# Optimization experiments

Hardware: AMD Instinct MI355X
Metric: run time of the kernel (lower is better)

The kernel has to match this reference:

```python
import jax, jax.numpy as jnp
import numpy as np

HEADS = 4

def _axial_attn(xs, wqkv, wproj, bproj, heads=HEADS):
    # xs: [B', C, L]; wqkv: [3C, C]; wproj: [C, C]; bproj: [C]
    Bp, C, L = xs.shape
    hd = C // heads
    scale = hd ** -0.5
    qkv = jnp.einsum('oc,bcl->bol', wqkv, xs)  # [B', 3C, L]
    q, k, v = jnp.split(qkv, 3, axis=1)
    q = q.reshape(Bp, heads, hd, L)
    k = k.reshape(Bp, heads, hd, L)
    v = v.reshape(Bp, heads, hd, L)
    attn = jax.nn.softmax(jnp.einsum('bhdi,bhdj->bhij', q, k) * scale, axis=-1)
    out = jnp.einsum('bhij,bhdj->bhdi', attn, v).reshape(Bp, C, L)
    return jnp.einsum('oc,bcl->bol', wproj, out) + bproj[None, :, None]

def setup_inputs() -> dict:
    key = jax.random.key(0)
    ks = jax.random.split(key, 7)
    B, C, H, W = 8, 128, 128, 128
    return {
        'x': jax.random.normal(ks[0], (B, C, H, W), dtype=jnp.float32),
        'wqkv_h': jax.random.normal(ks[1], (3 * C, C), dtype=jnp.float32) * 0.05,
        'wproj_h': jax.random.normal(ks[2], (C, C), dtype=jnp.float32) * 0.05,
        'bproj_h': jax.random.normal(ks[3], (C,), dtype=jnp.float32) * 0.05,
        'wqkv_w': jax.random.normal(ks[4], (3 * C, C), dtype=jnp.float32) * 0.05,
        'wproj_w': jax.random.normal(ks[5], (C, C), dtype=jnp.float32) * 0.05,
        'bproj_w': jax.random.normal(ks[6], (C,), dtype=jnp.float32) * 0.05,
    }

def reference(x, wqkv_h, wproj_h, bproj_h, wqkv_w, wproj_w, bproj_w):
    B, C, H, W = x.shape
    # height pass: rows become batch, attend along W
    xh = x.transpose(0, 2, 1, 3).reshape(B * H, C, W)
    xh = _axial_attn(xh, wqkv_h, wproj_h, bproj_h)
    xh = xh.reshape(B, H, C, W).transpose(0, 2, 1, 3)
    # width pass: cols become batch, attend along H
    xw = x.transpose(0, 3, 1, 2).reshape(B * W, C, H)
    xw = _axial_attn(xw, wqkv_w, wproj_w, bproj_w)
    xw = xw.reshape(B, W, C, H).transpose(0, 2, 3, 1)
    return (xh + xw) / 2
```

## Files before the change

### kernel.cpp

```cpp
#include <hip/hip_runtime.h>
#include <hip/hip_bf16.h>
#include <stdint.h>

typedef __attribute__((ext_vector_type(8))) short short8v;
typedef __attribute__((ext_vector_type(4))) float f32x4;
typedef unsigned short u16;
typedef unsigned int u32;

__device__ __align__(16) u16 g_xh [8u * 128u * 128u * 128u];
__device__ __align__(16) u16 g_xTw[8u * 128u * 128u * 128u];
__device__ __align__(16) u16 g_W1 [8u * 128u * 128u * 128u];
__device__ __align__(16) u16 g_W2 [8u * 128u * 128u * 128u];
__device__ __align__(16) u16 g_wqkvP[2u * 49152u];
__device__ __align__(16) u16 g_wpP [2u * 16384u];

#define XST_OFF 0
#define QT_OFF  32768
#define KT_OFF  43008
#define VH_OFF  53248
#define OT_OFF  61952
#define SMEM_BYTES 72192

__device__ __forceinline__ u16 f2bf(float f) {
    u32 b = __float_as_uint(f);
    b += 0x7FFFu + ((b >> 16) & 1u);
    return (u16)(b >> 16);
}
__device__ __forceinline__ u32 pk2(float a, float b) {
    __hip_bfloat162 h = __float22bfloat162_rn(make_float2(a, b));
    union { __hip_bfloat162 h; u32 u; } cv; cv.h = h; return cv.u;
}
__device__ __forceinline__ float bf2f(u16 u) {
    return __uint_as_float(((u32)u) << 16);
}

__global__ __launch_bounds__(512)
void prep_weights(const float* __restrict__ wqkv_h, const float* __restrict__ wproj_h,
                  const float* __restrict__ wqkv_w, const float* __restrict__ wproj_w)
{
    const float QSC = 0.17677669529663687f * 1.4426950408889634f;
    int id = blockIdx.x * 512 + threadIdx.x;
    if (id < 12288) {
        int p = id / 6144, i2 = id % 6144;
        int h = i2 / 1536, i3 = i2 % 1536;
        int t = i3 / 256,  i4 = i3 % 256;
        int kk = i4 / 64,  lane = i4 % 64;
        int cc = lane & 15, qq = lane >> 4;
        int r96 = t * 16 + cc;
        int g = r96 >> 5, rl = r96 & 31;
        const float* src = (p == 0 ? wqkv_h : wqkv_w) + (g * 128 + h * 32 + rl) * 128 + kk * 32 + qq * 8;
        float4 a = *(const float4*)src;
        float4 c = *(const float4*)(src + 4);
        float s = (g == 0) ? QSC : 1.0f;
        *(uint4*)(g_wqkvP + (size_t)id * 8) =
            make_uint4(pk2(a.x * s, a.y * s), pk2(a.z * s, a.w * s),
                       pk2(c.x * s, c.y * s), pk2(c.z * s, c.w * s));
    } else {
        int id2 = id - 12288;
        int p = id2 / 2048, i2 = id2 % 2048;
        int h = i2 / 512,  i3 = i2 % 512;
        int t = i3 / 64,   lane = i3 % 64;
        int cc = lane & 15, qq = lane >> 4;
        int o = t * 16 + cc;
        const float* src = (p == 0 ? wproj_h : wproj_w) + o * 128 + h * 32 + qq * 8;
        float4 a = *(const float4*)src;
        float4 c = *(const float4*)(src + 4);
        *(uint4*)(g_wpP + (size_t)id2 * 8) =
            make_uint4(pk2(a.x * 0.5f, a.y * 0.5f), pk2(a.z * 0.5f, a.w * 0.5f),
                       pk2(c.x * 0.5f, c.y * 0.5f), pk2(c.z * 0.5f, c.w * 0.5f));
    }
}

__global__ __launch_bounds__(256)
void transpose_x(const float* __restrict__ x)
{
    __shared__ char tsm[32768];
    const int b = blockIdx.x >> 6;
    const int hp = blockIdx.x & 63;
    const int tid = threadIdx.x;
    for (int hh = 0; hh < 2; ++hh) {
        const int h = hp * 2 + hh;
        #pragma unroll
        for (int it = 0; it < 16; ++it) {
            int task = it * 256 + tid;
            int w = task & 127, c4 = task >> 7;
            const float* p = x + (size_t)b * 2097152 + (c4 * 4) * 16384 + h * 128 + w;
            u32 u0 = pk2(p[0], p[16384]);
            u32 u1 = pk2(p[2 * 16384], p[3 * 16384]);
            int off = w * 256 + ((((c4 >> 1) << 4) ^ ((w & 7) << 4)) | ((c4 & 1) << 3));
            *(uint2*)(tsm + off) = make_uint2(u0, u1);
        }
        __syncthreads();
        #pragma unroll
        for (int it = 0; it < 8; ++it) {
            int i = it * 256 + tid;
            *(uint4*)(g_xh + (size_t)(b * 128 + h) * 16384 + i * 8) = *(const uint4*)(tsm + i * 16);
        }
        #pragma unroll
        for (int it = 0; it < 8; ++it) {
            int i = it * 256 + tid;
            int w = i >> 4, c8 = i & 15;
            uint4 v = *(const uint4*)(tsm + w * 256 + ((c8 << 4) ^ ((w & 7) << 4)));
            size_t ds = ((size_t)(b * 128 + w) * 128 + h) * 128 + (((c8 << 4) ^ ((h & 7) << 4)) >> 1);
            *(uint4*)(g_xTw + ds) = v;
        }
        __syncthreads();
    }
}

__global__ __launch_bounds__(512, 4)
void attn_kernel(const float* __restrict__ bias_h, const float* __restrict__ bias_w)
{
    extern __shared__ char smem[];
    const int t    = threadIdx.x;
    const int lane = t & 63;
    const int wv   = t >> 6;
    const int cc   = lane & 15;
    const int qq   = lane >> 4;
    const int pass = blockIdx.x >> 10;
    const int b    = (blockIdx.x >> 7) & 7;
    const int row  = blockIdx.x & 127;
    const f32x4 zf4 = (f32x4){0.f, 0.f, 0.f, 0.f};

    {
        const u16* slab = (pass ? g_xTw : g_xh) + (size_t)(b * 128 + row) * 16384;
        #pragma unroll
        for (int it = 0; it < 4; ++it) {
            int idx = t + 512 * it;
            *(uint4*)(smem + XST_OFF + idx * 16) = *(const uint4*)(slab + idx * 8);
        }
    }

    const float* bias = pass ? bias_w : bias_h;
    float biasr[4];
    #pragma unroll
    for (int r = 0; r < 4; ++r) biasr[r] = bias[wv * 16 + 4 * qq + r] * 0.5f;

    f32x4 yacc[8];
    #pragma unroll
    for (int i = 0; i < 8; ++i) yacc[i] = zf4;

    __syncthreads();

    const int og = wv & 1;
    const int lg = wv >> 1;

    for (int h = 0; h < 4; ++h) {
        const u16* wb  = g_wqkvP + (size_t)(pass * 4 + h) * 12288;
        const u16* wpb = g_wpP   + (size_t)(pass * 4 + h) * 4096 + (wv * 64 + lane) * 8;

        {
            f32x4 acc[3][2];
            #pragma unroll
            for (int ot = 0; ot < 3; ++ot)
                #pragma unroll
                for (int lt = 0; lt < 2; ++lt) acc[ot][lt] = zf4;
            __builtin_amdgcn_s_setprio(1);
            #pragma unroll
            for (int kk = 0; kk < 4; ++kk) {
                short8v A[3], Bf[2];
                #pragma unroll
                for (int ot = 0; ot < 3; ++ot)
                    A[ot] = *(const short8v*)(wb + (((og * 3 + ot) * 4 + kk) * 64 + lane) * 8);
                #pragma unroll
                for (int lt = 0; lt < 2; ++lt) {
                    int l = lg * 32 + lt * 16 + cc;
                    Bf[lt] = *(const short8v*)(smem + XST_OFF + l * 256 + (((kk * 64 + qq * 16)) ^ ((l & 7) << 4)));
                }
                #pragma unroll
                for (int ot = 0; ot < 3; ++ot)
                    #pragma unroll
                    for (int lt = 0; lt < 2; ++lt)
                        acc[ot][lt] = __builtin_amdgcn_mfma_f32_16x16x32_bf16(A[ot], Bf[lt], acc[ot][lt], 0, 0, 0);
            }
            __builtin_amdgcn_s_setprio(0);
            #pragma unroll
            for (int ot = 0; ot < 3; ++ot) {
                int got = og * 3 + ot;
                #pragma unroll
                for (int lt = 0; lt < 2; ++lt) {
                    int l0 = (lg * 2 + lt) * 16 + cc;
                    f32x4 v = acc[ot][lt];
                    if (got < 2) {
                        *(uint2*)(smem + QT_OFF + l0 * 80 + (got * 16 + 4 * qq) * 2) =
                            make_uint2(pk2(v[0], v[1]), pk2(v[2], v[3]));
                    } else if (got < 4) {
                        *(uint2*)(smem + KT_OFF + l0 * 80 + ((got - 2) * 16 + 4 * qq) * 2) =
                            make_uint2(pk2(v[0], v[1]), pk2(v[2], v[3]));
                    } else {
                        int d0 = (got - 4) * 16 + 4 * qq;
                        #pragma unroll
                        for (int r = 0; r < 4; ++r)
                            *(u16*)(smem + VH_OFF + (d0 + r) * 272 + l0 * 2) = f2bf(v[r]);
                    }
                }
            }
        }
        __syncthreads();

        f32x4 sacc[8];
        {
            short8v aq = *(const short8v*)(smem + QT_OFF + (wv * 16 + cc) * 80 + qq * 16);
            __builtin_amdgcn_s_setprio(1);
            #pragma unroll
            for (int jt = 0; jt < 8; ++jt) {
                short8v bk = *(const short8v*)(smem + KT_OFF + (jt * 16 + cc) * 80 + qq * 16);
                sacc[jt] = __builtin_amdgcn_mfma_f32_16x16x32_bf16(bk, aq, zf4, 0, 0, 0);
            }
            __builtin_amdgcn_s_setprio(0);
        }
        float mx = -3.4e38f;
        #pragma unroll
        for (int jt = 0; jt < 8; ++jt)
            #pragma unroll
            for (int r = 0; r < 4; ++r) mx = fmaxf(mx, sacc[jt][r]);
        mx = fmaxf(mx, __shfl_xor(mx, 16));
        mx = fmaxf(mx, __shfl_xor(mx, 32));
        float sm = 0.f;
        #pragma unroll
        for (int jt = 0; jt < 8; ++jt)
            #pragma unroll
            for (int r = 0; r < 4; ++r) {
                float p = exp2f(sacc[jt][r] - mx);
                sacc[jt][r] = p;
                sm += p;
            }
        sm += __shfl_xor(sm, 16);
        sm += __shfl_xor(sm, 32);
        float rden = 1.0f / sm;
        u32 u[8][2];
        #pragma unroll
        for (int jt = 0; jt < 8; ++jt) {
            u[jt][0] = pk2(sacc[jt][0], sacc[jt][1]);
            u[jt][1] = pk2(sacc[jt][2], sacc[jt][3]);
        }

        f32x4 oacc[2] = {zf4, zf4};
        const int base = cc + ((qq & 1) << 5);
        const bool hiT = (qq >> 1) != 0;
        __builtin_amdgcn_s_setprio(1);
        #pragma unroll
        for (int kt = 0; kt < 4; ++kt) {
            int a0 = __shfl((int)u[2 * kt][0], base),      a1 = __shfl((int)u[2 * kt][1], base);
            int a2 = __shfl((int)u[2 * kt][0], base + 16), a3 = __shfl((int)u[2 * kt][1], base + 16);
            int b0 = __shfl((int)u[2 * kt + 1][0], base),      b1 = __shfl((int)u[2 * kt + 1][1], base);
            int b2 = __shfl((int)u[2 * kt + 1][0], base + 16), b3 = __shfl((int)u[2 * kt + 1][1], base + 16);
            union { uint4 u4; short8v s8; } pf;
            pf.u4 = make_uint4((u32)(hiT ? b0 : a0), (u32)(hiT ? b1 : a1),
                               (u32)(hiT ? b2 : a2), (u32)(hiT ? b3 : a3));
            #pragma unroll
            for (int dt = 0; dt < 2; ++dt) {
                short8v vf = *(const short8v*)(smem + VH_OFF + (dt * 16 + cc) * 272 + kt * 64 + qq * 16);
                oacc[dt] = __builtin_amdgcn_mfma_f32_16x16x32_bf16(vf, pf.s8, oacc[dt], 0, 0, 0);
            }
        }
        __builtin_amdgcn_s_setprio(0);
        #pragma unroll
        for (int dt = 0; dt < 2; ++dt) {
            *(uint2*)(smem + OT_OFF + (wv * 16 + cc) * 80 + (dt * 16 + 4 * qq) * 2) =
                make_uint2(pk2(oacc[dt][0] * rden, oacc[dt][1] * rden),
                           pk2(oacc[dt][2] * rden, oacc[dt][3] * rden));
        }
        __syncthreads();

        {
            short8v aw = *(const short8v*)wpb;
            __builtin_amdgcn_s_setprio(1);
            #pragma unroll
            for (int it = 0; it < 8; ++it) {
                short8v of = *(const short8v*)(smem + OT_OFF + (it * 16 + cc) * 80 + qq * 16);
                yacc[it] = __builtin_amdgcn_mfma_f32_16x16x32_bf16(aw, of, yacc[it], 0, 0, 0);
            }
            __builtin_amdgcn_s_setprio(0);
        }
    }

    u16* dst = pass ? g_W2 : g_W1;
    #pragma unroll
    for (int it = 0; it < 8; ++it) {
        int l = it * 16 + cc;
        u32 p01 = pk2(yacc[it][0] + biasr[0], yacc[it][1] + biasr[1]);
        u32 p23 = pk2(yacc[it][2] + biasr[2], yacc[it][3] + biasr[3]);
        int o0 = wv * 16 + 4 * qq;
        size_t idx = ((size_t)(b * 128 + o0) * 128 + row) * 128 + l;
        dst[idx]         = (u16)p01;
        dst[idx + 16384] = (u16)(p01 >> 16);
        dst[idx + 32768] = (u16)p23;
        dst[idx + 49152] = (u16)(p23 >> 16);
    }
}

__global__ __launch_bounds__(256)
void merge_w(float* __restrict__ out)
{
    __shared__ char msm[128 * 264];
    const int b = blockIdx.x >> 7;
    const int o = blockIdx.x & 127;
    const int tid = threadIdx.x;
    const u16* slab = g_W2 + (size_t)(b * 128 + o) * 16384;
    #pragma unroll
    for (int it = 0; it < 8; ++it) {
        int i = it * 256 + tid;
        int w = i >> 4, h8 = i & 15;
        *(uint4*)(msm + w * 264 + h8 * 16) = *(const uint4*)(slab + w * 128 + h8 * 8);
    }
    __syncthreads();
    const u16* w1p = g_W1 + (size_t)(b * 128 + o) * 16384;
    float* op = out + (size_t)(b * 128 + o) * 16384;
    #pragma unroll
    for (int it = 0; it < 8; ++it) {
        int i = it * 256 + tid;
        int h = i >> 4, w8 = i & 15;
        uint4 w1 = *(const uint4*)(w1p + h * 128 + w8 * 8);
        float f[8];
        #pragma unroll
        for (int k = 0; k < 8; ++k)
            f[k] = bf2f(*(const u16*)(msm + (w8 * 8 + k) * 264 + h * 2));
        float* dp = op + h * 128 + w8 * 8;
        float4 v0, v1;
        v0.x = f[0] + bf2f((u16)(w1.x & 0xFFFF));
        v0.y = f[1] + bf2f((u16)(w1.x >> 16));
        v0.z = f[2] + bf2f((u16)(w1.y & 0xFFFF));
        v0.w = f[3] + bf2f((u16)(w1.y >> 16));
        v1.x = f[4] + bf2f((u16)(w1.z & 0xFFFF));
        v1.y = f[5] + bf2f((u16)(w1.z >> 16));
        v1.z = f[6] + bf2f((u16)(w1.w & 0xFFFF));
        v1.w = f[7] + bf2f((u16)(w1.w >> 16));
        *(float4*)dp = v0;
        *(float4*)(dp + 4) = v1;
    }
}

extern "C" void kernel_launch(void* const* d_in, const int* in_sizes, int n_in,
                              void* d_out, int out_size, void* d_ws, size_t ws_size,
                              hipStream_t stream)
{
    const float* x       = (const float*)d_in[0];
    const float* wqkv_h  = (const float*)d_in[1];
    const float* wproj_h = (const float*)d_in[2];
    const float* bproj_h = (const float*)d_in[3];
    const float* wqkv_w  = (const float*)d_in[4];
    const float* wproj_w = (const float*)d_in[5];
    const float* bproj_w = (const float*)d_in[6];
    float* out = (float*)d_out;

    (void)hipFuncSetAttribute((const void*)attn_kernel,
                              hipFuncAttributeMaxDynamicSharedMemorySize, SMEM_BYTES);

    prep_weights<<<dim3(32), dim3(512), 0, stream>>>(wqkv_h, wproj_h, wqkv_w, wproj_w);
    transpose_x<<<dim3(512), dim3(256), 0, stream>>>(x);
    attn_kernel<<<dim3(2048), dim3(512), SMEM_BYTES, stream>>>(bproj_h, bproj_w);
    merge_w<<<dim3(1024), dim3(256), 0, stream>>>(out);
}
```

Measured before the change: 168.2 us.

## Keep attention output in registers for projection, drop LDS staging buffer

The per-head attention output is no longer written to an LDS tile and read back across waves. Each wave now shuffles its own output into MFMA B-operand layout and projects it against all eight output-channel tiles of the projection weight, so every wave owns a fixed 16-column strip instead of 16 output channels. This removes the OT shared buffer, one barrier on the last head, and LDS traffic, and shrinks shared memory, which may allow higher occupancy. In exchange each wave loads eight weight fragments per head instead of one, and the bias is read per output tile at store time.

```diff
diff --git a/kernel.cpp b/kernel.cpp
--- a/kernel.cpp
+++ b/kernel.cpp
@@ -18,8 +18,7 @@
 #define QT_OFF  32768
 #define KT_OFF  43008
 #define VH_OFF  53248
-#define OT_OFF  61952
-#define SMEM_BYTES 72192
+#define SMEM_BYTES 61952
 
 __device__ __forceinline__ u16 f2bf(float f) {
     u32 b = __float_as_uint(f);
@@ -132,9 +131,6 @@
     }
 
     const float* bias = pass ? bias_w : bias_h;
-    float biasr[4];
-    #pragma unroll
-    for (int r = 0; r < 4; ++r) biasr[r] = bias[wv * 16 + 4 * qq + r] * 0.5f;
 
     f32x4 yacc[8];
     #pragma unroll
@@ -147,7 +143,7 @@
 
     for (int h = 0; h < 4; ++h) {
         const u16* wb  = g_wqkvP + (size_t)(pass * 4 + h) * 12288;
-        const u16* wpb = g_wpP   + (size_t)(pass * 4 + h) * 4096 + (wv * 64 + lane) * 8;
+        const u16* wpb = g_wpP   + (size_t)(pass * 4 + h) * 4096;
 
         {
             f32x4 acc[3][2];
@@ -255,33 +251,40 @@
             }
         }
         __builtin_amdgcn_s_setprio(0);
-        #pragma unroll
-        for (int dt = 0; dt < 2; ++dt) {
-            *(uint2*)(smem + OT_OFF + (wv * 16 + cc) * 80 + (dt * 16 + 4 * qq) * 2) =
-                make_uint2(pk2(oacc[dt][0] * rden, oacc[dt][1] * rden),
-                           pk2(oacc[dt][2] * rden, oacc[dt][3] * rden));
-        }
-        __syncthreads();
-
+
+        if (h < 3) __syncthreads();
+
+        union { uint4 u4; short8v s8; } of;
         {
-            short8v aw = *(const short8v*)wpb;
+            u32 o00 = pk2(oacc[0][0] * rden, oacc[0][1] * rden);
+            u32 o01 = pk2(oacc[0][2] * rden, oacc[0][3] * rden);
+            u32 o10 = pk2(oacc[1][0] * rden, oacc[1][1] * rden);
+            u32 o11 = pk2(oacc[1][2] * rden, oacc[1][3] * rden);
+            u32 a0 = (u32)__shfl((int)o00, base),      a1 = (u32)__shfl((int)o01, base);
+            u32 c0 = (u32)__shfl((int)o10, base),      c1 = (u32)__shfl((int)o11, base);
+            u32 b0 = (u32)__shfl((int)o00, base + 16), b1 = (u32)__shfl((int)o01, base + 16);
+            u32 d0 = (u32)__shfl((int)o10, base + 16), d1 = (u32)__shfl((int)o11, base + 16);
+            of.u4 = make_uint4(hiT ? c0 : a0, hiT ? c1 : a1, hiT ? d0 : b0, hiT ? d1 : b1);
+        }
+        {
             __builtin_amdgcn_s_setprio(1);
             #pragma unroll
-            for (int it = 0; it < 8; ++it) {
-                short8v of = *(const short8v*)(smem + OT_OFF + (it * 16 + cc) * 80 + qq * 16);
-                yacc[it] = __builtin_amdgcn_mfma_f32_16x16x32_bf16(aw, of, yacc[it], 0, 0, 0);
+            for (int ot = 0; ot < 8; ++ot) {
+                short8v aw = *(const short8v*)(wpb + ((size_t)(ot * 64 + lane)) * 8);
+                yacc[ot] = __builtin_amdgcn_mfma_f32_16x16x32_bf16(aw, of.s8, yacc[ot], 0, 0, 0);
             }
             __builtin_amdgcn_s_setprio(0);
         }
     }
 
     u16* dst = pass ? g_W2 : g_W1;
+    const int l = wv * 16 + cc;
     #pragma unroll
-    for (int it = 0; it < 8; ++it) {
-        int l = it * 16 + cc;
-        u32 p01 = pk2(yacc[it][0] + biasr[0], yacc[it][1] + biasr[1]);
-        u32 p23 = pk2(yacc[it][2] + biasr[2], yacc[it][3] + biasr[3]);
-        int o0 = wv * 16 + 4 * qq;
+    for (int ot = 0; ot < 8; ++ot) {
+        float4 bb = *(const float4*)(bias + ot * 16 + 4 * qq);
+        u32 p01 = pk2(yacc[ot][0] + bb.x * 0.5f, yacc[ot][1] + bb.y * 0.5f);
+        u32 p23 = pk2(yacc[ot][2] + bb.z * 0.5f, yacc[ot][3] + bb.w * 0.5f);
+        int o0 = ot * 16 + 4 * qq;
         size_t idx = ((size_t)(b * 128 + o0) * 128 + row) * 128 + l;
         dst[idx]         = (u16)p01;
         dst[idx + 16384] = (u16)(p01 >> 16);
```

After: 182.8 us. +8.7%, slower.
